# Optimization experiments

Hardware: AMD Instinct MI355X
Metric: run time of the kernel (lower is better)

The kernel has to match this reference:

```python
import jax, jax.numpy as jnp
import numpy as np

DEPTH = 16                      # complete binary tree depth (root level = DEPTH)
NUM_LEVELS = DEPTH + 1          # node_order in [0, DEPTH]
N_NODES = 2 ** (DEPTH + 1) - 1  # 131071
VOCAB = 50000
EMB = 128
HID = 128


def setup_inputs() -> dict:
    key = jax.random.key(0)
    ks = jax.random.split(key, 6)
    # --- deterministic complete binary tree structure ---
    idx = np.arange(N_NODES)
    depth = np.floor(np.log2(idx + 1)).astype(np.int64)  # root idx 0 has depth 0
    node_order = (DEPTH - depth).astype(np.int64)        # leaves evaluated first (order 0)
    internal = np.arange(2 ** DEPTH - 1)                 # nodes with children
    parents = np.repeat(internal, 2)                     # consecutive grouping per parent
    children = np.stack([2 * internal + 1, 2 * internal + 2], axis=1).ravel()
    adjacency_list = np.stack([parents, children], axis=1).astype(np.int64)
    edge_order = node_order[parents]
    s = 0.02
    return {
        "features": jax.random.randint(ks[0], (N_NODES,), 0, VOCAB),
        "node_order": jnp.asarray(node_order),
        "adjacency_list": jnp.asarray(adjacency_list),
        "edge_order": jnp.asarray(edge_order),
        "emb": jax.random.normal(ks[1], (VOCAB, EMB), jnp.float32) * s,
        "W_iou": jax.random.normal(ks[2], (EMB, 3 * HID), jnp.float32) * s,
        "b_iou": jnp.zeros((3 * HID,), jnp.float32),
        "U_iou": jax.random.normal(ks[3], (HID, 3 * HID), jnp.float32) * s,
        "W_f": jax.random.normal(ks[4], (EMB, HID), jnp.float32) * s,
        "b_f": jnp.zeros((HID,), jnp.float32),
        "U_f": jax.random.normal(ks[5], (HID, HID), jnp.float32) * s,
    }


def reference(features, node_order, adjacency_list, edge_order,
              emb, W_iou, b_iou, U_iou, W_f, b_f, U_f):
    x = emb[features]                                   # [N, EMB] embedding lookup
    par = adjacency_list[:, 0]                          # [E]
    chd = adjacency_list[:, 1]                          # [E]
    Wx = x @ W_iou + b_iou                              # [N, 3H] input contributions (precomputed)
    Wfx = x @ W_f + b_f                                 # [N, H] forget-gate input term
    N = x.shape[0]
    H = W_f.shape[1]
    h = jnp.zeros((N, H), x.dtype)
    c = jnp.zeros((N, H), x.dtype)
    # level-synchronous TreeLSTM: leaves (level 0) up to root
    for lvl in range(NUM_LEVELS):
        nmask = (node_order == lvl)[:, None]            # nodes updated this level
        emask = (edge_order == lvl)[:, None].astype(x.dtype)  # edges feeding them
        child_h = h[chd]                                # [E, H] gather children
        child_c = c[chd]
        h_sum = jax.ops.segment_sum(child_h * emask, par, num_segments=N)  # [N, H]
        iou = Wx + h_sum @ U_iou                        # [N, 3H]
        i, o, u = jnp.split(iou, 3, axis=1)
        i = jax.nn.sigmoid(i)
        o = jax.nn.sigmoid(o)
        u = jnp.tanh(u)
        f = jax.nn.sigmoid(Wfx[par] + child_h @ U_f)    # [E, H] per-edge forget gate
        c_sum = jax.ops.segment_sum(f * child_c * emask, par, num_segments=N)
        c_new = i * u + c_sum                           # level 0: c_sum == 0 -> i*u (leaf branch)
        c = jnp.where(nmask, c_new, c)
        h = jnp.where(nmask, o * jnp.tanh(c_new), h)
    return h, c
```

## Files before the change

kernel.cpp:

```cpp
#include <hip/hip_runtime.h>
#include <math.h>

#define NN 131071
#define HD 128
#define N_INTERNAL 65535
#define LEAF_BASE 65535

typedef short bf16x8 __attribute__((ext_vector_type(8)));
typedef unsigned short u16x8 __attribute__((ext_vector_type(8)));
typedef unsigned short u16x4 __attribute__((ext_vector_type(4)));
typedef float f32x4 __attribute__((ext_vector_type(4)));

__device__ __forceinline__ float sigm(float z) { return 1.0f / (1.0f + __expf(-z)); }
__device__ __forceinline__ float tanh_f(float z) { return 1.0f - 2.0f / (__expf(2.0f * z) + 1.0f); }

__device__ __forceinline__ unsigned short f2bf(float f) {
    unsigned u = __float_as_uint(f);
    u += 0x7FFFu + ((u >> 16) & 1u);
    return (unsigned short)(u >> 16);
}
__device__ __forceinline__ float bf2f(unsigned short b) {
    return __uint_as_float(((unsigned)b) << 16);
}

__device__ __forceinline__ f32x4 mfma16(bf16x8 a, bf16x8 b, f32x4 c) {
    return __builtin_amdgcn_mfma_f32_16x16x32_bf16(a, b, c, 0, 0, 0);
}

__device__ __forceinline__ float4 addf4(float4 a, float4 b) {
    float4 r; r.x = a.x + b.x; r.y = a.y + b.y; r.z = a.z + b.z; r.w = a.w + b.w; return r;
}

__device__ __forceinline__ bf16x8 pk8(float4 a, float4 b) {
    u16x8 p;
    p[0] = f2bf(a.x); p[1] = f2bf(a.y); p[2] = f2bf(a.z); p[3] = f2bf(a.w);
    p[4] = f2bf(b.x); p[5] = f2bf(b.y); p[6] = f2bf(b.z); p[7] = f2bf(b.w);
    return *(bf16x8*)&p;
}

__device__ __forceinline__ void lds_store8(unsigned short* region, int r, int cc, float4 a, float4 b) {
    u16x8 p;
    p[0] = f2bf(a.x); p[1] = f2bf(a.y); p[2] = f2bf(a.z); p[3] = f2bf(a.w);
    p[4] = f2bf(b.x); p[5] = f2bf(b.y); p[6] = f2bf(b.z); p[7] = f2bf(b.w);
    *(u16x8*)&region[r * HD + ((cc ^ (r & 7)) << 3)] = p;
}

__device__ __forceinline__ bf16x8 lds_frag(const unsigned short* region, int row, int ks, int kl) {
    int cc = ks * 4 + kl;
    return *(const bf16x8*)&region[row * HD + ((cc ^ (row & 7)) << 3)];
}

__device__ __forceinline__ bf16x8 frag2(const unsigned short* M, int ct, int ks, int lane) {
    return *(const bf16x8*)&M[(((ct * 4 + ks) * 64) + lane) * 8];
}

__global__ __launch_bounds__(256) void build_packed(
    const float* __restrict__ W_iou, const float* __restrict__ U_iou,
    const float* __restrict__ W_f, const float* __restrict__ U_f,
    unsigned short* __restrict__ ws)
{
    int f = blockIdx.x * 256 + threadIdx.x;
    int mat = f >> 13;
    int rem = f & 8191;
    int ct = rem >> 8;
    int ks = (rem >> 6) & 3;
    int lane = rem & 63;
    int col = ct * 16 + (lane & 15);
    int k0 = ks * 32 + (lane >> 4) * 8;
    u16x8 out;
#pragma unroll
    for (int e = 0; e < 8; ++e) {
        int k = k0 + e;
        float v;
        if (mat == 0) v = (col < 384) ? W_iou[k * 384 + col] : W_f[k * HD + (col - 384)];
        else          v = (col < 384) ? U_iou[k * 384 + col] : U_f[k * HD + (col - 384)];
        out[e] = f2bf(v);
    }
    *(u16x8*)&ws[(size_t)f * 8] = out;
}

__global__ __launch_bounds__(512) void xp_leaf_kernel(
    const int* __restrict__ feat, const float* __restrict__ emb,
    const unsigned short* __restrict__ WT2,
    const float* __restrict__ b_iou, const float* __restrict__ b_f,
    unsigned short* __restrict__ XPb, float* __restrict__ hbuf, float* __restrict__ cbuf)
{
    __shared__ unsigned short ldsx[64 * HD];
    const int t = threadIdx.x;
    const int m0 = blockIdx.x * 64;
    {
        int r = t >> 3, c8 = t & 7;
        int n = m0 + r;
        int nn = n < NN ? n : 0;
        const float* sx = emb + (size_t)feat[nn] * HD + c8 * 16;
        float4 x0 = *(const float4*)(sx + 0);
        float4 x1 = *(const float4*)(sx + 4);
        float4 x2 = *(const float4*)(sx + 8);
        float4 x3 = *(const float4*)(sx + 12);
        lds_store8(ldsx, r, c8 * 2 + 0, x0, x1);
        lds_store8(ldsx, r, c8 * 2 + 1, x2, x3);
    }
    __syncthreads();

    const int lane = t & 63, w = t >> 6;
    const int jq = w & 3, mh = w >> 2;
    const int l15 = lane & 15, kl = lane >> 4;

    f32x4 zero = {0.f, 0.f, 0.f, 0.f};
    f32x4 acc[4][2][2];
#pragma unroll
    for (int g = 0; g < 4; ++g)
#pragma unroll
        for (int mp = 0; mp < 2; ++mp)
#pragma unroll
            for (int jt = 0; jt < 2; ++jt) acc[g][mp][jt] = zero;

#pragma unroll
    for (int ks = 0; ks < 4; ++ks) {
        bf16x8 a0 = lds_frag(ldsx, (mh * 2 + 0) * 16 + l15, ks, kl);
        bf16x8 a1 = lds_frag(ldsx, (mh * 2 + 1) * 16 + l15, ks, kl);
#pragma unroll
        for (int g = 0; g < 4; ++g) {
#pragma unroll
            for (int jt = 0; jt < 2; ++jt) {
                bf16x8 b = frag2(WT2, g * 8 + jq * 2 + jt, ks, lane);
                acc[g][0][jt] = mfma16(a0, b, acc[g][0][jt]);
                acc[g][1][jt] = mfma16(a1, b, acc[g][1][jt]);
            }
        }
    }

#pragma unroll
    for (int mp = 0; mp < 2; ++mp) {
#pragma unroll
        for (int jt = 0; jt < 2; ++jt) {
            int j = jq * 32 + jt * 16 + l15;
            int nb = m0 + (mh * 2 + mp) * 16 + kl * 4;
            float bi = b_iou[j], bo = b_iou[HD + j], bu = b_iou[2 * HD + j], bf = b_f[j];
#pragma unroll
            for (int r = 0; r < 4; ++r) {
                int n = nb + r;
                if (n >= NN) continue;
                if (n >= LEAF_BASE) {
                    float iv = sigm(acc[0][mp][jt][r] + bi);
                    float ov = sigm(acc[1][mp][jt][r] + bo);
                    float uv = tanh_f(acc[2][mp][jt][r] + bu);
                    float cv = iv * uv;
                    cbuf[(size_t)n * HD + j] = cv;
                    hbuf[(size_t)n * HD + j] = ov * tanh_f(cv);
                } else {
                    u16x4 pk;
                    pk[0] = f2bf(acc[0][mp][jt][r] + bi);
                    pk[1] = f2bf(acc[1][mp][jt][r] + bo);
                    pk[2] = f2bf(acc[2][mp][jt][r] + bu);
                    pk[3] = f2bf(acc[3][mp][jt][r] + bf);
                    *(u16x4*)&XPb[((size_t)n * HD + j) * 4] = pk;
                }
            }
        }
    }
}

__device__ __forceinline__ void level_body(
    unsigned short* lds,
    const unsigned short* __restrict__ UT2, const unsigned short* __restrict__ XPb,
    float* __restrict__ hbuf, float* __restrict__ cbuf, int base, int count, int m0)
{
    unsigned short* ldshs = lds;
    unsigned short* ldsh1 = lds + 8192;
    unsigned short* ldsh2 = lds + 16384;

    const int t = threadIdx.x;
    {
        int r = t >> 3, c8 = t & 7;
        int row = m0 + r;
        int n = base + (row < count ? row : 0);
        const float* s1 = hbuf + (size_t)(2 * n + 1) * HD + c8 * 16;
        const float* s2 = hbuf + (size_t)(2 * n + 2) * HD + c8 * 16;
        float4 p0 = *(const float4*)(s1 + 0);
        float4 p1 = *(const float4*)(s1 + 4);
        float4 p2 = *(const float4*)(s1 + 8);
        float4 p3 = *(const float4*)(s1 + 12);
        float4 q0 = *(const float4*)(s2 + 0);
        float4 q1 = *(const float4*)(s2 + 4);
        float4 q2 = *(const float4*)(s2 + 8);
        float4 q3 = *(const float4*)(s2 + 12);
        lds_store8(ldsh1, r, c8 * 2 + 0, p0, p1);
        lds_store8(ldsh1, r, c8 * 2 + 1, p2, p3);
        lds_store8(ldsh2, r, c8 * 2 + 0, q0, q1);
        lds_store8(ldsh2, r, c8 * 2 + 1, q2, q3);
        lds_store8(ldshs, r, c8 * 2 + 0, addf4(p0, q0), addf4(p1, q1));
        lds_store8(ldshs, r, c8 * 2 + 1, addf4(p2, q2), addf4(p3, q3));
    }
    __syncthreads();

    const int lane = t & 63, w = t >> 6;
    const int jq = w & 3, mh = w >> 2;
    const int l15 = lane & 15, kl = lane >> 4;

    f32x4 zero = {0.f, 0.f, 0.f, 0.f};
    f32x4 acc[5][2][2];
#pragma unroll
    for (int g = 0; g < 5; ++g)
#pragma unroll
        for (int mp = 0; mp < 2; ++mp)
#pragma unroll
            for (int jt = 0; jt < 2; ++jt) acc[g][mp][jt] = zero;

#pragma unroll
    for (int ks = 0; ks < 4; ++ks) {
        bf16x8 ahs0 = lds_frag(ldshs, (mh * 2 + 0) * 16 + l15, ks, kl);
        bf16x8 ahs1 = lds_frag(ldshs, (mh * 2 + 1) * 16 + l15, ks, kl);
        bf16x8 ah10 = lds_frag(ldsh1, (mh * 2 + 0) * 16 + l15, ks, kl);
        bf16x8 ah11 = lds_frag(ldsh1, (mh * 2 + 1) * 16 + l15, ks, kl);
        bf16x8 ah20 = lds_frag(ldsh2, (mh * 2 + 0) * 16 + l15, ks, kl);
        bf16x8 ah21 = lds_frag(ldsh2, (mh * 2 + 1) * 16 + l15, ks, kl);
#pragma unroll
        for (int jt = 0; jt < 2; ++jt) {
            bf16x8 Bi = frag2(UT2,  0 + jq * 2 + jt, ks, lane);
            bf16x8 Bo = frag2(UT2,  8 + jq * 2 + jt, ks, lane);
            bf16x8 Bu = frag2(UT2, 16 + jq * 2 + jt, ks, lane);
            bf16x8 Bf = frag2(UT2, 24 + jq * 2 + jt, ks, lane);
            acc[0][0][jt] = mfma16(ahs0, Bi, acc[0][0][jt]);
            acc[0][1][jt] = mfma16(ahs1, Bi, acc[0][1][jt]);
            acc[1][0][jt] = mfma16(ahs0, Bo, acc[1][0][jt]);
            acc[1][1][jt] = mfma16(ahs1, Bo, acc[1][1][jt]);
            acc[2][0][jt] = mfma16(ahs0, Bu, acc[2][0][jt]);
            acc[2][1][jt] = mfma16(ahs1, Bu, acc[2][1][jt]);
            acc[3][0][jt] = mfma16(ah10, Bf, acc[3][0][jt]);
            acc[3][1][jt] = mfma16(ah11, Bf, acc[3][1][jt]);
            acc[4][0][jt] = mfma16(ah20, Bf, acc[4][0][jt]);
            acc[4][1][jt] = mfma16(ah21, Bf, acc[4][1][jt]);
        }
    }

#pragma unroll
    for (int mp = 0; mp < 2; ++mp) {
#pragma unroll
        for (int jt = 0; jt < 2; ++jt) {
            int j = jq * 32 + jt * 16 + l15;
#pragma unroll
            for (int r = 0; r < 4; ++r) {
                int row = m0 + (mh * 2 + mp) * 16 + kl * 4 + r;
                if (row >= count) continue;
                int n = base + row;
                u16x4 pk = *(const u16x4*)&XPb[((size_t)n * HD + j) * 4];
                float iv = sigm(acc[0][mp][jt][r] + bf2f(pk[0]));
                float ov = sigm(acc[1][mp][jt][r] + bf2f(pk[1]));
                float uv = tanh_f(acc[2][mp][jt][r] + bf2f(pk[2]));
                float fx = bf2f(pk[3]);
                float f1 = sigm(acc[3][mp][jt][r] + fx);
                float f2 = sigm(acc[4][mp][jt][r] + fx);
                float c1 = cbuf[(size_t)(2 * n + 1) * HD + j];
                float c2 = cbuf[(size_t)(2 * n + 2) * HD + j];
                float cn = fmaf(iv, uv, fmaf(f1, c1, f2 * c2));
                cbuf[(size_t)n * HD + j] = cn;
                hbuf[(size_t)n * HD + j] = ov * tanh_f(cn);
            }
        }
    }
}

__global__ __launch_bounds__(512) void level_u_kernel(
    const unsigned short* __restrict__ UT2, const unsigned short* __restrict__ XPb,
    float* __restrict__ hbuf, float* __restrict__ cbuf, int base, int count)
{
    __shared__ unsigned short lds[3 * 64 * HD];
    level_body(lds, UT2, XPb, hbuf, cbuf, base, count, blockIdx.x * 64);
}

__global__ __launch_bounds__(512) void tail_kernel3(
    const unsigned short* __restrict__ UT2, const unsigned short* __restrict__ XPb,
    float* __restrict__ hbuf, float* __restrict__ cbuf)
{
    __shared__ unsigned short hlds[255 * HD];
    const int t = threadIdx.x;

    {
        int n = 127 + (t >> 2);
        int c0 = (t & 3) * 32;
        const float* src = hbuf + (size_t)n * HD + c0;
#pragma unroll
        for (int q = 0; q < 4; ++q) {
            float4 a = *(const float4*)(src + q * 8);
            float4 b = *(const float4*)(src + q * 8 + 4);
            int cc = (c0 >> 3) + q;
            *(bf16x8*)&hlds[n * HD + ((cc ^ (n & 7)) << 3)] = pk8(a, b);
        }
    }
    __syncthreads();

    const int lane = t & 63, w = t >> 6;
    const int jq = w & 3, mh = w >> 2;
    const int l15 = lane & 15, kl = lane >> 4;

#pragma unroll 1
    for (int lvl = 10; lvl <= 16; ++lvl) {
        const int count = 1 << (16 - lvl);
        const int base = count - 1;
        if (mh * 32 < count) {
            f32x4 zero = {0.f, 0.f, 0.f, 0.f};
            f32x4 acc[5][2][2];
#pragma unroll
            for (int g = 0; g < 5; ++g)
#pragma unroll
                for (int mp = 0; mp < 2; ++mp)
#pragma unroll
                    for (int jt = 0; jt < 2; ++jt) acc[g][mp][jt] = zero;

#pragma unroll
            for (int ks = 0; ks < 4; ++ks) {
                bf16x8 ah1[2], ah2[2];
#pragma unroll
                for (int mp = 0; mp < 2; ++mp) {
                    int row = mh * 32 + mp * 16 + l15;
                    int rr = row < count ? row : count - 1;
                    int n = base + rr;
                    ah1[mp] = lds_frag(hlds, 2 * n + 1, ks, kl);
                    ah2[mp] = lds_frag(hlds, 2 * n + 2, ks, kl);
                }
#pragma unroll
                for (int jt = 0; jt < 2; ++jt) {
                    bf16x8 Bi = frag2(UT2,  0 + jq * 2 + jt, ks, lane);
                    bf16x8 Bo = frag2(UT2,  8 + jq * 2 + jt, ks, lane);
                    bf16x8 Bu = frag2(UT2, 16 + jq * 2 + jt, ks, lane);
                    bf16x8 Bf = frag2(UT2, 24 + jq * 2 + jt, ks, lane);
#pragma unroll
                    for (int mp = 0; mp < 2; ++mp) {
                        acc[0][mp][jt] = mfma16(ah1[mp], Bi, mfma16(ah2[mp], Bi, acc[0][mp][jt]));
                        acc[1][mp][jt] = mfma16(ah1[mp], Bo, mfma16(ah2[mp], Bo, acc[1][mp][jt]));
                        acc[2][mp][jt] = mfma16(ah1[mp], Bu, mfma16(ah2[mp], Bu, acc[2][mp][jt]));
                        acc[3][mp][jt] = mfma16(ah1[mp], Bf, acc[3][mp][jt]);
                        acc[4][mp][jt] = mfma16(ah2[mp], Bf, acc[4][mp][jt]);
                    }
                }
            }

#pragma unroll
            for (int mp = 0; mp < 2; ++mp) {
#pragma unroll
                for (int jt = 0; jt < 2; ++jt) {
                    int j = jq * 32 + jt * 16 + l15;
#pragma unroll
                    for (int r = 0; r < 4; ++r) {
                        int row = mh * 32 + mp * 16 + kl * 4 + r;
                        if (row >= count) continue;
                        int n = base + row;
                        u16x4 pk = *(const u16x4*)&XPb[((size_t)n * HD + j) * 4];
                        float iv = sigm(acc[0][mp][jt][r] + bf2f(pk[0]));
                        float ov = sigm(acc[1][mp][jt][r] + bf2f(pk[1]));
                        float uv = tanh_f(acc[2][mp][jt][r] + bf2f(pk[2]));
                        float fx = bf2f(pk[3]);
                        float f1 = sigm(acc[3][mp][jt][r] + fx);
                        float f2 = sigm(acc[4][mp][jt][r] + fx);
                        float c1 = cbuf[(size_t)(2 * n + 1) * HD + j];
                        float c2 = cbuf[(size_t)(2 * n + 2) * HD + j];
                        float cn = fmaf(iv, uv, fmaf(f1, c1, f2 * c2));
                        float hn = ov * tanh_f(cn);
                        cbuf[(size_t)n * HD + j] = cn;
                        hbuf[(size_t)n * HD + j] = hn;
                        int cc = j >> 3;
                        hlds[n * HD + ((cc ^ (n & 7)) << 3) + (j & 7)] = f2bf(hn);
                    }
                }
            }
        }
        __syncthreads();
    }
}

template <int MT>
__global__ __launch_bounds__(128) void leaf_kernel(
    const int* __restrict__ feat, const float* __restrict__ emb,
    const float* __restrict__ W_iou, const float* __restrict__ b_iou,
    float* __restrict__ hbuf, float* __restrict__ cbuf, int base)
{
    __shared__ float X[MT][HD];
    const int j = threadIdx.x;
    const int m0 = blockIdx.x * MT;
#pragma unroll
    for (int m = 0; m < MT; ++m) {
        int n = base + m0 + m;
        X[m][j] = emb[(size_t)feat[n] * HD + j];
    }
    __syncthreads();
    float ai[MT], ao[MT], au[MT];
#pragma unroll
    for (int m = 0; m < MT; ++m) {
        ai[m] = b_iou[j]; ao[m] = b_iou[HD + j]; au[m] = b_iou[2 * HD + j];
    }
#pragma unroll 4
    for (int k = 0; k < HD; ++k) {
        float wi = W_iou[k * 3 * HD + j];
        float wo = W_iou[k * 3 * HD + HD + j];
        float wu = W_iou[k * 3 * HD + 2 * HD + j];
#pragma unroll
        for (int m = 0; m < MT; ++m) {
            float x = X[m][k];
            ai[m] = fmaf(x, wi, ai[m]); ao[m] = fmaf(x, wo, ao[m]); au[m] = fmaf(x, wu, au[m]);
        }
    }
#pragma unroll
    for (int m = 0; m < MT; ++m) {
        int n = base + m0 + m;
        float iv = sigm(ai[m]); float ov = sigm(ao[m]); float uv = tanh_f(au[m]);
        float cv = iv * uv;
        cbuf[(size_t)n * HD + j] = cv;
        hbuf[(size_t)n * HD + j] = ov * tanh_f(cv);
    }
}

template <int MT>
__global__ __launch_bounds__(128) void level_kernel(
    const int* __restrict__ feat, const float* __restrict__ emb,
    const float* __restrict__ W_iou, const float* __restrict__ b_iou,
    const float* __restrict__ U_iou,
    const float* __restrict__ W_f, const float* __restrict__ b_f,
    const float* __restrict__ U_f,
    float* __restrict__ hbuf, float* __restrict__ cbuf, int base)
{
    __shared__ float X[MT][HD];
    __shared__ float H1[MT][HD];
    __shared__ float H2[MT][HD];
    const int j = threadIdx.x;
    const int m0 = blockIdx.x * MT;
#pragma unroll
    for (int m = 0; m < MT; ++m) {
        int n = base + m0 + m;
        X[m][j]  = emb[(size_t)feat[n] * HD + j];
        H1[m][j] = hbuf[(size_t)(2 * n + 1) * HD + j];
        H2[m][j] = hbuf[(size_t)(2 * n + 2) * HD + j];
    }
    __syncthreads();
    float ai[MT], ao[MT], au[MT], g1[MT], g2[MT];
#pragma unroll
    for (int m = 0; m < MT; ++m) {
        ai[m] = b_iou[j]; ao[m] = b_iou[HD + j]; au[m] = b_iou[2 * HD + j];
        g1[m] = b_f[j]; g2[m] = b_f[j];
    }
#pragma unroll 2
    for (int k = 0; k < HD; ++k) {
        float wi = W_iou[k * 3 * HD + j];
        float wo = W_iou[k * 3 * HD + HD + j];
        float wu = W_iou[k * 3 * HD + 2 * HD + j];
        float ui = U_iou[k * 3 * HD + j];
        float uo = U_iou[k * 3 * HD + HD + j];
        float uu = U_iou[k * 3 * HD + 2 * HD + j];
        float wf = W_f[k * HD + j];
        float uf = U_f[k * HD + j];
#pragma unroll
        for (int m = 0; m < MT; ++m) {
            float x = X[m][k]; float h1 = H1[m][k]; float h2 = H2[m][k]; float hs = h1 + h2;
            ai[m] = fmaf(x, wi, fmaf(hs, ui, ai[m]));
            ao[m] = fmaf(x, wo, fmaf(hs, uo, ao[m]));
            au[m] = fmaf(x, wu, fmaf(hs, uu, au[m]));
            g1[m] = fmaf(x, wf, fmaf(h1, uf, g1[m]));
            g2[m] = fmaf(x, wf, fmaf(h2, uf, g2[m]));
        }
    }
#pragma unroll
    for (int m = 0; m < MT; ++m) {
        int n = base + m0 + m;
        float iv = sigm(ai[m]); float ov = sigm(ao[m]); float uv = tanh_f(au[m]);
        float f1 = sigm(g1[m]); float f2 = sigm(g2[m]);
        float c1 = cbuf[(size_t)(2 * n + 1) * HD + j];
        float c2 = cbuf[(size_t)(2 * n + 2) * HD + j];
        float cn = fmaf(iv, uv, fmaf(f1, c1, f2 * c2));
        cbuf[(size_t)n * HD + j] = cn;
        hbuf[(size_t)n * HD + j] = ov * tanh_f(cn);
    }
}

extern "C" void kernel_launch(void* const* d_in, const int* in_sizes, int n_in,
                              void* d_out, int out_size, void* d_ws, size_t ws_size,
                              hipStream_t stream)
{
    const int*   feat  = (const int*)d_in[0];
    const float* emb   = (const float*)d_in[4];
    const float* W_iou = (const float*)d_in[5];
    const float* b_iou = (const float*)d_in[6];
    const float* U_iou = (const float*)d_in[7];
    const float* W_f   = (const float*)d_in[8];
    const float* b_f   = (const float*)d_in[9];
    const float* U_f   = (const float*)d_in[10];

    float* hbuf = (float*)d_out;
    float* cbuf = hbuf + (size_t)NN * HD;

    const size_t PACK_BYTES = 2u * 65536u * 2u;
    const size_t XP_BYTES   = (size_t)N_INTERNAL * HD * 4 * 2;
    if (ws_size >= PACK_BYTES + XP_BYTES) {
        unsigned short* wpk = (unsigned short*)d_ws;
        const unsigned short* WT2 = wpk;
        const unsigned short* UT2 = wpk + 65536;
        unsigned short* XPb = (unsigned short*)((char*)d_ws + PACK_BYTES);

        build_packed<<<64, 256, 0, stream>>>(W_iou, U_iou, W_f, U_f, wpk);
        xp_leaf_kernel<<<2048, 512, 0, stream>>>(feat, emb, WT2, b_iou, b_f, XPb, hbuf, cbuf);

        for (int lvl = 1; lvl <= 9; ++lvl) {
            const int count = 1 << (16 - lvl);
            const int base  = count - 1;
            level_u_kernel<<<count / 64, 512, 0, stream>>>(UT2, XPb, hbuf, cbuf, base, count);
        }
        tail_kernel3<<<1, 512, 0, stream>>>(UT2, XPb, hbuf, cbuf);
    } else {
        leaf_kernel<16><<<65536 / 16, 128, 0, stream>>>(feat, emb, W_iou, b_iou, hbuf, cbuf, 65535);
        for (int lvl = 1; lvl <= 16; ++lvl) {
            const int d = 16 - lvl;
            const int count = 1 << d;
            const int base = count - 1;
            if (count >= 16) {
                level_kernel<16><<<count / 16, 128, 0, stream>>>(
                    feat, emb, W_iou, b_iou, U_iou, W_f, b_f, U_f, hbuf, cbuf, base);
            } else if (count == 8) {
                level_kernel<8><<<1, 128, 0, stream>>>(
                    feat, emb, W_iou, b_iou, U_iou, W_f, b_f, U_f, hbuf, cbuf, base);
            } else if (count == 4) {
                level_kernel<4><<<1, 128, 0, stream>>>(
                    feat, emb, W_iou, b_iou, U_iou, W_f, b_f, U_f, hbuf, cbuf, base);
            } else if (count == 2) {
                level_kernel<2><<<1, 128, 0, stream>>>(
                    feat, emb, W_iou, b_iou, U_iou, W_f, b_f, U_f, hbuf, cbuf, base);
            } else {
                level_kernel<1><<<1, 128, 0, stream>>>(
                    feat, emb, W_iou, b_iou, U_iou, W_f, b_f, U_f, hbuf, cbuf, base);
            }
        }
    }
}
```

Baseline: 290.7 us.

## Keep bf16 copies of embeddings and hidden states; load MFMA fragments directly from global

Adds a pass converting the embedding table to bf16 and keeps a bf16 shadow of h written by the leaf and level kernels. The leaf and level kernels load MFMA A-fragments straight from these bf16 rows instead of staging fp32 data through LDS with a barrier. The child-sum GEMM is replaced by two accumulating MFMAs per child, which adds MFMA work. The extra conversion pass over the full vocabulary table and the additional bf16 writes trade against the halved gather traffic.

```diff
diff --git a/kernel.cpp b/kernel.cpp
--- a/kernel.cpp
+++ b/kernel.cpp
@@ -38,13 +38,6 @@
     return *(bf16x8*)&p;
 }
 
-__device__ __forceinline__ void lds_store8(unsigned short* region, int r, int cc, float4 a, float4 b) {
-    u16x8 p;
-    p[0] = f2bf(a.x); p[1] = f2bf(a.y); p[2] = f2bf(a.z); p[3] = f2bf(a.w);
-    p[4] = f2bf(b.x); p[5] = f2bf(b.y); p[6] = f2bf(b.z); p[7] = f2bf(b.w);
-    *(u16x8*)&region[r * HD + ((cc ^ (r & 7)) << 3)] = p;
-}
-
 __device__ __forceinline__ bf16x8 lds_frag(const unsigned short* region, int row, int ks, int kl) {
     int cc = ks * 4 + kl;
     return *(const bf16x8*)&region[row * HD + ((cc ^ (row & 7)) << 3)];
@@ -52,6 +45,10 @@
 
 __device__ __forceinline__ bf16x8 frag2(const unsigned short* M, int ct, int ks, int lane) {
     return *(const bf16x8*)&M[(((ct * 4 + ks) * 64) + lane) * 8];
+}
+
+__device__ __forceinline__ bf16x8 row_frag(const unsigned short* rowp, int ks, int kl) {
+    return *(const bf16x8*)&rowp[ks * 32 + kl * 8];
 }
 
 __global__ __launch_bounds__(256) void build_packed(
@@ -79,33 +76,34 @@
     *(u16x8*)&ws[(size_t)f * 8] = out;
 }
 
-__global__ __launch_bounds__(512) void xp_leaf_kernel(
-    const int* __restrict__ feat, const float* __restrict__ emb,
+__global__ __launch_bounds__(256) void conv_emb(
+    const float* __restrict__ emb, unsigned short* __restrict__ emb16)
+{
+    size_t idx = ((size_t)blockIdx.x * 256 + threadIdx.x) * 8;
+    float4 a = *(const float4*)(emb + idx);
+    float4 b = *(const float4*)(emb + idx + 4);
+    bf16x8 v = pk8(a, b);
+    *(bf16x8*)&emb16[idx] = v;
+}
+
+__global__ __launch_bounds__(512) void xp_leaf2(
+    const int* __restrict__ feat, const unsigned short* __restrict__ emb16,
     const unsigned short* __restrict__ WT2,
     const float* __restrict__ b_iou, const float* __restrict__ b_f,
-    unsigned short* __restrict__ XPb, float* __restrict__ hbuf, float* __restrict__ cbuf)
-{
-    __shared__ unsigned short ldsx[64 * HD];
+    unsigned short* __restrict__ XPb, unsigned short* __restrict__ hb16,
+    float* __restrict__ hbuf, float* __restrict__ cbuf)
+{
     const int t = threadIdx.x;
     const int m0 = blockIdx.x * 64;
-    {
-        int r = t >> 3, c8 = t & 7;
-        int n = m0 + r;
-        int nn = n < NN ? n : 0;
-        const float* sx = emb + (size_t)feat[nn] * HD + c8 * 16;
-        float4 x0 = *(const float4*)(sx + 0);
-        float4 x1 = *(const float4*)(sx + 4);
-        float4 x2 = *(const float4*)(sx + 8);
-        float4 x3 = *(const float4*)(sx + 12);
-        lds_store8(ldsx, r, c8 * 2 + 0, x0, x1);
-        lds_store8(ldsx, r, c8 * 2 + 1, x2, x3);
-    }
-    __syncthreads();
-
     const int lane = t & 63, w = t >> 6;
     const int jq = w & 3, mh = w >> 2;
     const int l15 = lane & 15, kl = lane >> 4;
 
+    int na0 = m0 + (mh * 2 + 0) * 16 + l15;
+    int na1 = m0 + (mh * 2 + 1) * 16 + l15;
+    const unsigned short* x0p = emb16 + (size_t)feat[na0 < NN ? na0 : NN - 1] * HD;
+    const unsigned short* x1p = emb16 + (size_t)feat[na1 < NN ? na1 : NN - 1] * HD;
+
     f32x4 zero = {0.f, 0.f, 0.f, 0.f};
     f32x4 acc[4][2][2];
 #pragma unroll
@@ -117,8 +115,8 @@
 
 #pragma unroll
     for (int ks = 0; ks < 4; ++ks) {
-        bf16x8 a0 = lds_frag(ldsx, (mh * 2 + 0) * 16 + l15, ks, kl);
-        bf16x8 a1 = lds_frag(ldsx, (mh * 2 + 1) * 16 + l15, ks, kl);
+        bf16x8 a0 = row_frag(x0p, ks, kl);
+        bf16x8 a1 = row_frag(x1p, ks, kl);
 #pragma unroll
         for (int g = 0; g < 4; ++g) {
 #pragma unroll
@@ -146,8 +144,10 @@
                     float ov = sigm(acc[1][mp][jt][r] + bo);
                     float uv = tanh_f(acc[2][mp][jt][r] + bu);
                     float cv = iv * uv;
+                    float hv = ov * tanh_f(cv);
                     cbuf[(size_t)n * HD + j] = cv;
-                    hbuf[(size_t)n * HD + j] = ov * tanh_f(cv);
+                    hbuf[(size_t)n * HD + j] = hv;
+                    hb16[(size_t)n * HD + j] = f2bf(hv);
                 } else {
                     u16x4 pk;
                     pk[0] = f2bf(acc[0][mp][jt][r] + bi);
@@ -161,43 +161,26 @@
     }
 }
 
-__device__ __forceinline__ void level_body(
-    unsigned short* lds,
+__global__ __launch_bounds__(512) void level_u2(
     const unsigned short* __restrict__ UT2, const unsigned short* __restrict__ XPb,
-    float* __restrict__ hbuf, float* __restrict__ cbuf, int base, int count, int m0)
-{
-    unsigned short* ldshs = lds;
-    unsigned short* ldsh1 = lds + 8192;
-    unsigned short* ldsh2 = lds + 16384;
-
+    const unsigned short* __restrict__ hb16_c, unsigned short* __restrict__ hb16,
+    float* __restrict__ hbuf, float* __restrict__ cbuf, int base)
+{
     const int t = threadIdx.x;
-    {
-        int r = t >> 3, c8 = t & 7;
-        int row = m0 + r;
-        int n = base + (row < count ? row : 0);
-        const float* s1 = hbuf + (size_t)(2 * n + 1) * HD + c8 * 16;
-        const float* s2 = hbuf + (size_t)(2 * n + 2) * HD + c8 * 16;
-        float4 p0 = *(const float4*)(s1 + 0);
-        float4 p1 = *(const float4*)(s1 + 4);
-        float4 p2 = *(const float4*)(s1 + 8);
-        float4 p3 = *(const float4*)(s1 + 12);
-        float4 q0 = *(const float4*)(s2 + 0);
-        float4 q1 = *(const float4*)(s2 + 4);
-        float4 q2 = *(const float4*)(s2 + 8);
-        float4 q3 = *(const float4*)(s2 + 12);
-        lds_store8(ldsh1, r, c8 * 2 + 0, p0, p1);
-        lds_store8(ldsh1, r, c8 * 2 + 1, p2, p3);
-        lds_store8(ldsh2, r, c8 * 2 + 0, q0, q1);
-        lds_store8(ldsh2, r, c8 * 2 + 1, q2, q3);
-        lds_store8(ldshs, r, c8 * 2 + 0, addf4(p0, q0), addf4(p1, q1));
-        lds_store8(ldshs, r, c8 * 2 + 1, addf4(p2, q2), addf4(p3, q3));
-    }
-    __syncthreads();
-
+    const int m0 = blockIdx.x * 64;
     const int lane = t & 63, w = t >> 6;
     const int jq = w & 3, mh = w >> 2;
     const int l15 = lane & 15, kl = lane >> 4;
 
+    const unsigned short* c1p[2];
+    const unsigned short* c2p[2];
+#pragma unroll
+    for (int mp = 0; mp < 2; ++mp) {
+        int n = base + m0 + (mh * 2 + mp) * 16 + l15;
+        c1p[mp] = hb16_c + (size_t)(2 * n + 1) * HD;
+        c2p[mp] = hb16_c + (size_t)(2 * n + 2) * HD;
+    }
+
     f32x4 zero = {0.f, 0.f, 0.f, 0.f};
     f32x4 acc[5][2][2];
 #pragma unroll
@@ -209,28 +192,26 @@
 
 #pragma unroll
     for (int ks = 0; ks < 4; ++ks) {
-        bf16x8 ahs0 = lds_frag(ldshs, (mh * 2 + 0) * 16 + l15, ks, kl);
-        bf16x8 ahs1 = lds_frag(ldshs, (mh * 2 + 1) * 16 + l15, ks, kl);
-        bf16x8 ah10 = lds_frag(ldsh1, (mh * 2 + 0) * 16 + l15, ks, kl);
-        bf16x8 ah11 = lds_frag(ldsh1, (mh * 2 + 1) * 16 + l15, ks, kl);
-        bf16x8 ah20 = lds_frag(ldsh2, (mh * 2 + 0) * 16 + l15, ks, kl);
-        bf16x8 ah21 = lds_frag(ldsh2, (mh * 2 + 1) * 16 + l15, ks, kl);
+        bf16x8 ah1[2], ah2[2];
+#pragma unroll
+        for (int mp = 0; mp < 2; ++mp) {
+            ah1[mp] = row_frag(c1p[mp], ks, kl);
+            ah2[mp] = row_frag(c2p[mp], ks, kl);
+        }
 #pragma unroll
         for (int jt = 0; jt < 2; ++jt) {
             bf16x8 Bi = frag2(UT2,  0 + jq * 2 + jt, ks, lane);
             bf16x8 Bo = frag2(UT2,  8 + jq * 2 + jt, ks, lane);
             bf16x8 Bu = frag2(UT2, 16 + jq * 2 + jt, ks, lane);
             bf16x8 Bf = frag2(UT2, 24 + jq * 2 + jt, ks, lane);
-            acc[0][0][jt] = mfma16(ahs0, Bi, acc[0][0][jt]);
-            acc[0][1][jt] = mfma16(ahs1, Bi, acc[0][1][jt]);
-            acc[1][0][jt] = mfma16(ahs0, Bo, acc[1][0][jt]);
-            acc[1][1][jt] = mfma16(ahs1, Bo, acc[1][1][jt]);
-            acc[2][0][jt] = mfma16(ahs0, Bu, acc[2][0][jt]);
-            acc[2][1][jt] = mfma16(ahs1, Bu, acc[2][1][jt]);
-            acc[3][0][jt] = mfma16(ah10, Bf, acc[3][0][jt]);
-            acc[3][1][jt] = mfma16(ah11, Bf, acc[3][1][jt]);
-            acc[4][0][jt] = mfma16(ah20, Bf, acc[4][0][jt]);
-            acc[4][1][jt] = mfma16(ah21, Bf, acc[4][1][jt]);
+#pragma unroll
+            for (int mp = 0; mp < 2; ++mp) {
+                acc[0][mp][jt] = mfma16(ah1[mp], Bi, mfma16(ah2[mp], Bi, acc[0][mp][jt]));
+                acc[1][mp][jt] = mfma16(ah1[mp], Bo, mfma16(ah2[mp], Bo, acc[1][mp][jt]));
+                acc[2][mp][jt] = mfma16(ah1[mp], Bu, mfma16(ah2[mp], Bu, acc[2][mp][jt]));
+                acc[3][mp][jt] = mfma16(ah1[mp], Bf, acc[3][mp][jt]);
+                acc[4][mp][jt] = mfma16(ah2[mp], Bf, acc[4][mp][jt]);
+            }
         }
     }
 
@@ -241,9 +222,7 @@
             int j = jq * 32 + jt * 16 + l15;
 #pragma unroll
             for (int r = 0; r < 4; ++r) {
-                int row = m0 + (mh * 2 + mp) * 16 + kl * 4 + r;
-                if (row >= count) continue;
-                int n = base + row;
+                int n = base + m0 + (mh * 2 + mp) * 16 + kl * 4 + r;
                 u16x4 pk = *(const u16x4*)&XPb[((size_t)n * HD + j) * 4];
                 float iv = sigm(acc[0][mp][jt][r] + bf2f(pk[0]));
                 float ov = sigm(acc[1][mp][jt][r] + bf2f(pk[1]));
@@ -254,19 +233,13 @@
                 float c1 = cbuf[(size_t)(2 * n + 1) * HD + j];
                 float c2 = cbuf[(size_t)(2 * n + 2) * HD + j];
                 float cn = fmaf(iv, uv, fmaf(f1, c1, f2 * c2));
+                float hn = ov * tanh_f(cn);
                 cbuf[(size_t)n * HD + j] = cn;
-                hbuf[(size_t)n * HD + j] = ov * tanh_f(cn);
-            }
-        }
-    }
-}
-
-__global__ __launch_bounds__(512) void level_u_kernel(
-    const unsigned short* __restrict__ UT2, const unsigned short* __restrict__ XPb,
-    float* __restrict__ hbuf, float* __restrict__ cbuf, int base, int count)
-{
-    __shared__ unsigned short lds[3 * 64 * HD];
-    level_body(lds, UT2, XPb, hbuf, cbuf, base, count, blockIdx.x * 64);
+                hbuf[(size_t)n * HD + j] = hn;
+                hb16[(size_t)n * HD + j] = f2bf(hn);
+            }
+        }
+    }
 }
 
 __global__ __launch_bounds__(512) void tail_kernel3(
@@ -285,7 +258,8 @@
             float4 a = *(const float4*)(src + q * 8);
             float4 b = *(const float4*)(src + q * 8 + 4);
             int cc = (c0 >> 3) + q;
-            *(bf16x8*)&hlds[n * HD + ((cc ^ (n & 7)) << 3)] = pk8(a, b);
+            bf16x8 v = pk8(a, b);
+            *(bf16x8*)&hlds[n * HD + ((cc ^ (n & 7)) << 3)] = v;
         }
     }
     __syncthreads();
@@ -489,19 +463,25 @@
 
     const size_t PACK_BYTES = 2u * 65536u * 2u;
     const size_t XP_BYTES   = (size_t)N_INTERNAL * HD * 4 * 2;
-    if (ws_size >= PACK_BYTES + XP_BYTES) {
+    const size_t HB_BYTES   = (size_t)131072 * HD * 2;
+    const size_t EMB_BYTES  = (size_t)50000 * HD * 2;
+    if (ws_size >= PACK_BYTES + XP_BYTES + HB_BYTES + EMB_BYTES) {
         unsigned short* wpk = (unsigned short*)d_ws;
         const unsigned short* WT2 = wpk;
         const unsigned short* UT2 = wpk + 65536;
-        unsigned short* XPb = (unsigned short*)((char*)d_ws + PACK_BYTES);
+        unsigned short* XPb  = (unsigned short*)((char*)d_ws + PACK_BYTES);
+        unsigned short* hb16 = (unsigned short*)((char*)d_ws + PACK_BYTES + XP_BYTES);
+        unsigned short* emb16= (unsigned short*)((char*)d_ws + PACK_BYTES + XP_BYTES + HB_BYTES);
 
         build_packed<<<64, 256, 0, stream>>>(W_iou, U_iou, W_f, U_f, wpk);
-        xp_leaf_kernel<<<2048, 512, 0, stream>>>(feat, emb, WT2, b_iou, b_f, XPb, hbuf, cbuf);
+        conv_emb<<<3125, 256, 0, stream>>>(emb, emb16);
+
+        xp_leaf2<<<2048, 512, 0, stream>>>(feat, emb16, WT2, b_iou, b_f, XPb, hb16, hbuf, cbuf);
 
         for (int lvl = 1; lvl <= 9; ++lvl) {
             const int count = 1 << (16 - lvl);
             const int base  = count - 1;
-            level_u_kernel<<<count / 64, 512, 0, stream>>>(UT2, XPb, hbuf, cbuf, base, count);
+            level_u2<<<count / 64, 512, 0, stream>>>(UT2, XPb, hb16, hb16, hbuf, cbuf, base);
         }
         tail_kernel3<<<1, 512, 0, stream>>>(UT2, XPb, hbuf, cbuf);
     } else {
```

Measured after the change: 326.9 us. +12.4%, slower.
